# Optimization experiments

Measured on AMD Instinct MI355X. Metric: run time of the kernel, lower is better.

The kernel has to match this reference:

```python
import jax, jax.numpy as jnp
from jax import lax
import numpy as np

B, T, F = 2048, 1000, 40
H1, H2 = 8, 6


def _p(key, shape, fan):
    # uniform(-1/sqrt(fan), 1/sqrt(fan)) like torch LSTM/Linear init
    bound = 1.0 / np.sqrt(fan)
    return jax.random.uniform(key, shape, jnp.float32, -bound, bound)


def setup_inputs() -> dict:
    key = jax.random.key(0)
    ks = jax.random.split(key, 11)
    return {
        "x": jax.random.normal(ks[0], (B, T, F), jnp.float32),
        "W_ih1": _p(ks[1], (4 * H1, F), H1),
        "W_hh1": _p(ks[2], (4 * H1, H1), H1),
        "b_ih1": _p(ks[3], (4 * H1,), H1),
        "b_hh1": _p(ks[4], (4 * H1,), H1),
        "W_ih2": _p(ks[5], (4 * H2, H1), H2),
        "W_hh2": _p(ks[6], (4 * H2, H2), H2),
        "b_ih2": _p(ks[7], (4 * H2,), H2),
        "b_hh2": _p(ks[8], (4 * H2,), H2),
        "W_fc": _p(ks[9], (1, H2), H2),
        "b_fc": _p(ks[10], (1,), H2),
    }


def lstm_layer(x, W_ih, W_hh, b_ih, b_hh):
    """batch_first unidirectional LSTM; returns all hidden states [B,T,H]."""
    Bb = x.shape[0]
    H = W_hh.shape[1]
    # precompute input-side gate preactivations for all timesteps: [T,B,4H]
    xg = (jnp.einsum('btf,gf->btg', x, W_ih) + b_ih + b_hh).transpose(1, 0, 2)
    W_hh_T = W_hh.T  # [H,4H]

    def step(carry, xg_t):
        h, c = carry
        g = xg_t + h @ W_hh_T  # [B,4H]
        i, f, gcell, o = jnp.split(g, 4, axis=-1)  # torch gate order i,f,g,o
        i = jax.nn.sigmoid(i)
        f = jax.nn.sigmoid(f)
        gcell = jnp.tanh(gcell)
        o = jax.nn.sigmoid(o)
        c = f * c + i * gcell
        h = o * jnp.tanh(c)
        return (h, c), h

    h0 = jnp.zeros((Bb, H), x.dtype)
    c0 = jnp.zeros((Bb, H), x.dtype)
    _, hs = lax.scan(step, (h0, c0), xg)  # hs: [T,B,H]
    return hs.transpose(1, 0, 2)


def reference(x, W_ih1, W_hh1, b_ih1, b_hh1, W_ih2, W_hh2, b_ih2, b_hh2, W_fc, b_fc):
    out = lstm_layer(x, W_ih1, W_hh1, b_ih1, b_hh1)
    out = jnp.tanh(out)
    out = lstm_layer(out, W_ih2, W_hh2, b_ih2, b_hh2)
    out = jnp.tanh(out)
    last = out[:, -1, :]  # [B,H2]
    logits = last @ W_fc.T + b_fc  # [B,1]
    return jax.nn.sigmoid(logits)
```

## Files before the change

### kernel.cpp

```cpp
#include <hip/hip_runtime.h>


constexpr int Bn = 2048, Tn = 1000, Fn = 40;
constexpr int H1n = 8, H2n = 6;
constexpr int TT  = 20;
constexpr int NTt = Tn / TT;
constexpr int BW  = 8;

constexpr int SROWF  = TT * Fn + 4;
constexpr int SXF    = BW * SROWF;
constexpr int SXB    = SXF * 4;
constexpr int NCHUNK = (SXB + 1023) / 1024;

__device__ __forceinline__ float frcp(float x) { return __builtin_amdgcn_rcpf(x); }
__device__ __forceinline__ float fsig(float x) { return frcp(1.0f + __expf(-x)); }
__device__ __forceinline__ float ftanh(float x) {
    return fmaf(2.0f, frcp(1.0f + __expf(-2.0f * x)), -1.0f);
}

template <int K>
__device__ __forceinline__ float bswz(float v) {
    return __int_as_float(__builtin_amdgcn_ds_swizzle(__float_as_int(v), (K << 5) | 0x18));
}

__global__ __launch_bounds__(256, 1) void lstm_upl(
    const float* __restrict__ x,
    const float* __restrict__ W_ih1, const float* __restrict__ W_hh1,
    const float* __restrict__ b_ih1, const float* __restrict__ b_hh1,
    const float* __restrict__ W_ih2, const float* __restrict__ W_hh2,
    const float* __restrict__ b_ih2, const float* __restrict__ b_hh2,
    const float* __restrict__ W_fc,  const float* __restrict__ b_fc,
    float* __restrict__ out)
{
    __shared__ float s_x [2][SXF];
    __shared__ float s_xg[2][TT * BW * 32];

    const int lane  = threadIdx.x & 63;
    const int wslot = __builtin_amdgcn_readfirstlane((int)(threadIdx.x >> 6));
    const int b0    = blockIdx.x * BW;


    if (wslot == 0) {
        const int q  = lane >> 3;
        const int j  = lane & 7;
        const int j2 = (j < H2n) ? j : (H2n - 1);

        float wi1[H1n], wf1[H1n], wg1[H1n], wo1[H1n];
#pragma unroll
        for (int k = 0; k < H1n; ++k) {
            wi1[k] = W_hh1[(     j) * H1n + k];
            wf1[k] = W_hh1[( 8 + j) * H1n + k];
            wg1[k] = W_hh1[(16 + j) * H1n + k];
            wo1[k] = W_hh1[(24 + j) * H1n + k];
        }
        float wi2[H1n], wf2[H1n], wg2[H1n], wo2[H1n];
#pragma unroll
        for (int k = 0; k < H1n; ++k) {
            wi2[k] = W_ih2[(     j2) * H1n + k];
            wf2[k] = W_ih2[( 6 + j2) * H1n + k];
            wg2[k] = W_ih2[(12 + j2) * H1n + k];
            wo2[k] = W_ih2[(18 + j2) * H1n + k];
        }
        float vi2[H2n], vf2[H2n], vg2[H2n], vo2[H2n];
#pragma unroll
        for (int k = 0; k < H2n; ++k) {
            vi2[k] = W_hh2[(     j2) * H2n + k];
            vf2[k] = W_hh2[( 6 + j2) * H2n + k];
            vg2[k] = W_hh2[(12 + j2) * H2n + k];
            vo2[k] = W_hh2[(18 + j2) * H2n + k];
        }
        const float bi2c = b_ih2[     j2] + b_hh2[     j2];
        const float bf2c = b_ih2[ 6 + j2] + b_hh2[ 6 + j2];
        const float bg2c = b_ih2[12 + j2] + b_hh2[12 + j2];
        const float bo2c = b_ih2[18 + j2] + b_hh2[18 + j2];

        float wfc[H2n];
#pragma unroll
        for (int k = 0; k < H2n; ++k) wfc[k] = W_fc[k];
        const float bfc = b_fc[0];

        float c1 = 0.f, c2 = 0.f;
        float h1s[H1n], th1s[H1n], h2s[H2n];
#pragma unroll
        for (int k = 0; k < H1n; ++k) { h1s[k] = 0.f; th1s[k] = 0.f; }
#pragma unroll
        for (int k = 0; k < H2n; ++k) h2s[k] = 0.f;

        const int myoff = q * 32 + j * 4;

        for (int p = 0; p <= NTt + 1; ++p) {
            if (p >= 2) {
                const float* xgt = &s_xg[(p - 2) & 1][0];
                float4 xg4 = *(const float4*)(xgt + myoff);
                for (int i = 0; i < TT; ++i) {
                    const int in = (i + 1 < TT) ? (i + 1) : i;
                    const float4 xgn = *(const float4*)(xgt + in * (BW * 32) + myoff);

                    float ai0 = xg4.x, ai1 = 0.f, af0 = xg4.y, af1 = 0.f;
                    float ag0 = xg4.z, ag1 = 0.f, ao0 = xg4.w, ao1 = 0.f;
#pragma unroll
                    for (int k = 0; k < H1n; k += 2) {
                        ai0 = fmaf(h1s[k], wi1[k], ai0); ai1 = fmaf(h1s[k+1], wi1[k+1], ai1);
                        af0 = fmaf(h1s[k], wf1[k], af0); af1 = fmaf(h1s[k+1], wf1[k+1], af1);
                        ag0 = fmaf(h1s[k], wg1[k], ag0); ag1 = fmaf(h1s[k+1], wg1[k+1], ag1);
                        ao0 = fmaf(h1s[k], wo1[k], ao0); ao1 = fmaf(h1s[k+1], wo1[k+1], ao1);
                    }
                    const float iv = fsig (ai0 + ai1);
                    const float fv = fsig (af0 + af1);
                    const float gv = ftanh(ag0 + ag1);
                    const float ov = fsig (ao0 + ao1);
                    c1 = fmaf(fv, c1, iv * gv);
                    const float h1v  = ov * ftanh(c1);
                    const float th1v = ftanh(h1v);

                    h1s[0] = bswz<0>(h1v); h1s[1] = bswz<1>(h1v);
                    h1s[2] = bswz<2>(h1v); h1s[3] = bswz<3>(h1v);
                    h1s[4] = bswz<4>(h1v); h1s[5] = bswz<5>(h1v);
                    h1s[6] = bswz<6>(h1v); h1s[7] = bswz<7>(h1v);
                    th1s[0] = bswz<0>(th1v); th1s[1] = bswz<1>(th1v);
                    th1s[2] = bswz<2>(th1v); th1s[3] = bswz<3>(th1v);
                    th1s[4] = bswz<4>(th1v); th1s[5] = bswz<5>(th1v);
                    th1s[6] = bswz<6>(th1v); th1s[7] = bswz<7>(th1v);

                    float bi0 = bi2c, bi1 = 0.f, bf0 = bf2c, bf1 = 0.f;
                    float bg0 = bg2c, bg1 = 0.f, bo0 = bo2c, bo1 = 0.f;
#pragma unroll
                    for (int k = 0; k < H2n; k += 2) {
                        bi0 = fmaf(h2s[k], vi2[k], bi0); bi1 = fmaf(h2s[k+1], vi2[k+1], bi1);
                        bf0 = fmaf(h2s[k], vf2[k], bf0); bf1 = fmaf(h2s[k+1], vf2[k+1], bf1);
                        bg0 = fmaf(h2s[k], vg2[k], bg0); bg1 = fmaf(h2s[k+1], vg2[k+1], bg1);
                        bo0 = fmaf(h2s[k], vo2[k], bo0); bo1 = fmaf(h2s[k+1], vo2[k+1], bo1);
                    }
#pragma unroll
                    for (int k = 0; k < H1n; k += 2) {
                        bi0 = fmaf(th1s[k], wi2[k], bi0); bi1 = fmaf(th1s[k+1], wi2[k+1], bi1);
                        bf0 = fmaf(th1s[k], wf2[k], bf0); bf1 = fmaf(th1s[k+1], wf2[k+1], bf1);
                        bg0 = fmaf(th1s[k], wg2[k], bg0); bg1 = fmaf(th1s[k+1], wg2[k+1], bg1);
                        bo0 = fmaf(th1s[k], wo2[k], bo0); bo1 = fmaf(th1s[k+1], wo2[k+1], bo1);
                    }
                    const float i2v = fsig (bi0 + bi1);
                    const float f2v = fsig (bf0 + bf1);
                    const float g2v = ftanh(bg0 + bg1);
                    const float o2v = fsig (bo0 + bo1);
                    c2 = fmaf(f2v, c2, i2v * g2v);
                    const float h2v = o2v * ftanh(c2);

                    h2s[0] = bswz<0>(h2v); h2s[1] = bswz<1>(h2v);
                    h2s[2] = bswz<2>(h2v); h2s[3] = bswz<3>(h2v);
                    h2s[4] = bswz<4>(h2v); h2s[5] = bswz<5>(h2v);

                    xg4 = xgn;
                }
            }
            __syncthreads();
        }

        if (j == 0) {
            float a = bfc;
#pragma unroll
            for (int k = 0; k < H2n; ++k) a = fmaf(ftanh(h2s[k]), wfc[k], a);
            out[b0 + q] = fsig(a);
        }
    } else {
        const int wp = wslot - 1;
        const int q  = lane >> 3;
        const int j  = lane & 7;

        float wI[Fn], wF[Fn], wG[Fn], wO[Fn];
#pragma unroll
        for (int k = 0; k < Fn; ++k) {
            wI[k] = W_ih1[(     j) * Fn + k];
            wF[k] = W_ih1[( 8 + j) * Fn + k];
            wG[k] = W_ih1[(16 + j) * Fn + k];
            wO[k] = W_ih1[(24 + j) * Fn + k];
        }
        const float bI = b_ih1[     j] + b_hh1[     j];
        const float bF = b_ih1[ 8 + j] + b_hh1[ 8 + j];
        const float bG = b_ih1[16 + j] + b_hh1[16 + j];
        const float bO = b_ih1[24 + j] + b_hh1[24 + j];

        const char* xcb = (const char*)x;

        for (int p = 0; p <= NTt + 1; ++p) {
            float4 vv[9];
            if (p < NTt) {
#pragma unroll
                for (int ci = 0; ci < 9; ++ci) {
                    const int c = wp + ci * 3;
                    if (c < NCHUNK) {
                        const int o = c * 1024 + lane * 16;
                        if (o < SXB) {
                            const int qq  = o / (SROWF * 4);
                            int       rem = o - qq * (SROWF * 4);
                            if (rem > TT * Fn * 4 - 16) rem = TT * Fn * 4 - 16;
                            vv[ci] = *(const float4*)(xcb
                                       + (size_t)(b0 + qq) * (Tn * Fn * 4)
                                       + (size_t)p * (TT * Fn * 4) + rem);
                        }
                    }
                }
            }

            if (p >= 1 && p <= NTt) {
                const float* xq = &s_x[(p - 1) & 1][0] + q * SROWF;
                float*       so = &s_xg[(p - 1) & 1][0];
                for (int r = wp; r < TT; r += 3) {
                    const float* xr = xq + r * Fn;
                    float i0 = bI, i1 = 0.f, i2 = 0.f, i3 = 0.f;
                    float f0 = bF, f1 = 0.f, f2 = 0.f, f3 = 0.f;
                    float g0 = bG, g1 = 0.f, g2 = 0.f, g3 = 0.f;
                    float o0 = bO, o1 = 0.f, o2 = 0.f, o3 = 0.f;
#pragma unroll
                    for (int k = 0; k < Fn; k += 4) {
                        const float4 cv = *(const float4*)&xr[k];
                        i0 = fmaf(cv.x, wI[k],     i0); i1 = fmaf(cv.y, wI[k + 1], i1);
                        i2 = fmaf(cv.z, wI[k + 2], i2); i3 = fmaf(cv.w, wI[k + 3], i3);
                        f0 = fmaf(cv.x, wF[k],     f0); f1 = fmaf(cv.y, wF[k + 1], f1);
                        f2 = fmaf(cv.z, wF[k + 2], f2); f3 = fmaf(cv.w, wF[k + 3], f3);
                        g0 = fmaf(cv.x, wG[k],     g0); g1 = fmaf(cv.y, wG[k + 1], g1);
                        g2 = fmaf(cv.z, wG[k + 2], g2); g3 = fmaf(cv.w, wG[k + 3], g3);
                        o0 = fmaf(cv.x, wO[k],     o0); o1 = fmaf(cv.y, wO[k + 1], o1);
                        o2 = fmaf(cv.z, wO[k + 2], o2); o3 = fmaf(cv.w, wO[k + 3], o3);
                    }
                    float4 r4;
                    r4.x = (i0 + i1) + (i2 + i3);
                    r4.y = (f0 + f1) + (f2 + f3);
                    r4.z = (g0 + g1) + (g2 + g3);
                    r4.w = (o0 + o1) + (o2 + o3);
                    *(float4*)&so[(r * BW + q) * 32 + j * 4] = r4;
                }
            }

            if (p < NTt) {
                char* ld = (char*)&s_x[p & 1][0];
#pragma unroll
                for (int ci = 0; ci < 9; ++ci) {
                    const int c = wp + ci * 3;
                    if (c < NCHUNK) {
                        const int o = c * 1024 + lane * 16;
                        if (o < SXB) *(float4*)(ld + o) = vv[ci];
                    }
                }
            }
            __syncthreads();
        }
    }
}

extern "C" void kernel_launch(void* const* d_in, const int* in_sizes, int n_in,
                              void* d_out, int out_size, void* d_ws, size_t ws_size,
                              hipStream_t stream) {
    (void)in_sizes; (void)n_in; (void)out_size; (void)d_ws; (void)ws_size;
    const float* x     = (const float*)d_in[0];
    const float* W_ih1 = (const float*)d_in[1];
    const float* W_hh1 = (const float*)d_in[2];
    const float* b_ih1 = (const float*)d_in[3];
    const float* b_hh1 = (const float*)d_in[4];
    const float* W_ih2 = (const float*)d_in[5];
    const float* W_hh2 = (const float*)d_in[6];
    const float* b_ih2 = (const float*)d_in[7];
    const float* b_hh2 = (const float*)d_in[8];
    const float* W_fc  = (const float*)d_in[9];
    const float* b_fc  = (const float*)d_in[10];
    float* out = (float*)d_out;

    lstm_upl<<<dim3(Bn / BW), dim3(256), 0, stream>>>(x, W_ih1, W_hh1, b_ih1, b_hh1,
                                                      W_ih2, W_hh2, b_ih2, b_hh2,
                                                      W_fc, b_fc, out);
}
```

Before: 727.9 us.

## Split LSTM layers across two waves with a shared-memory pipeline stage

The serial recurrence wave is split in two. One wave runs layer 1 and writes tanh(h1) per tile into a new double-buffered shared array, and a second wave runs layer 2 one tile behind. This shortens the per-timestep critical path of each wave, since the layer-1 and layer-2 recurrences now run concurrently. The cost is one fewer producer wave for the input projection (each now loads 13 chunks instead of 9), one more pipeline stage, and extra shared memory.

After: 854.2 us. 17.4% more time.

```diff
diff --git a/kernel.cpp b/kernel.cpp
--- a/kernel.cpp
+++ b/kernel.cpp
@@ -34,6 +34,7 @@
 {
     __shared__ float s_x [2][SXF];
     __shared__ float s_xg[2][TT * BW * 32];
+    __shared__ float s_t1[2][TT * BW * H1n];
 
     const int lane  = threadIdx.x & 63;
     const int wslot = __builtin_amdgcn_readfirstlane((int)(threadIdx.x >> 6));
@@ -41,9 +42,8 @@
 
 
     if (wslot == 0) {
-        const int q  = lane >> 3;
-        const int j  = lane & 7;
-        const int j2 = (j < H2n) ? j : (H2n - 1);
+        const int q = lane >> 3;
+        const int j = lane & 7;
 
         float wi1[H1n], wf1[H1n], wg1[H1n], wo1[H1n];
 #pragma unroll
@@ -53,6 +53,57 @@
             wg1[k] = W_hh1[(16 + j) * H1n + k];
             wo1[k] = W_hh1[(24 + j) * H1n + k];
         }
+
+        float c1 = 0.f;
+        float h1s[H1n];
+#pragma unroll
+        for (int k = 0; k < H1n; ++k) h1s[k] = 0.f;
+
+        const int myoff = q * 32 + j * 4;
+
+        for (int p = 0; p <= NTt + 2; ++p) {
+            if (p >= 2 && p <= NTt + 1) {
+                const int tile = p - 2;
+                const float* xgt = &s_xg[tile & 1][0];
+                float*       t1o = &s_t1[tile & 1][0];
+                float4 xg4 = *(const float4*)(xgt + myoff);
+                for (int i = 0; i < TT; ++i) {
+                    const int in = (i + 1 < TT) ? (i + 1) : i;
+                    const float4 xgn = *(const float4*)(xgt + in * (BW * 32) + myoff);
+
+                    float ai0 = xg4.x, ai1 = 0.f, af0 = xg4.y, af1 = 0.f;
+                    float ag0 = xg4.z, ag1 = 0.f, ao0 = xg4.w, ao1 = 0.f;
+#pragma unroll
+                    for (int k = 0; k < H1n; k += 2) {
+                        ai0 = fmaf(h1s[k], wi1[k], ai0); ai1 = fmaf(h1s[k+1], wi1[k+1], ai1);
+                        af0 = fmaf(h1s[k], wf1[k], af0); af1 = fmaf(h1s[k+1], wf1[k+1], af1);
+                        ag0 = fmaf(h1s[k], wg1[k], ag0); ag1 = fmaf(h1s[k+1], wg1[k+1], ag1);
+                        ao0 = fmaf(h1s[k], wo1[k], ao0); ao1 = fmaf(h1s[k+1], wo1[k+1], ao1);
+                    }
+                    const float iv = fsig (ai0 + ai1);
+                    const float fv = fsig (af0 + af1);
+                    const float gv = ftanh(ag0 + ag1);
+                    const float ov = fsig (ao0 + ao1);
+                    c1 = fmaf(fv, c1, iv * gv);
+                    const float h1v = ov * ftanh(c1);
+
+                    h1s[0] = bswz<0>(h1v); h1s[1] = bswz<1>(h1v);
+                    h1s[2] = bswz<2>(h1v); h1s[3] = bswz<3>(h1v);
+                    h1s[4] = bswz<4>(h1v); h1s[5] = bswz<5>(h1v);
+                    h1s[6] = bswz<6>(h1v); h1s[7] = bswz<7>(h1v);
+
+                    t1o[i * (BW * H1n) + q * H1n + j] = ftanh(h1v);
+
+                    xg4 = xgn;
+                }
+            }
+            __syncthreads();
+        }
+    } else if (wslot == 1) {
+        const int q  = lane >> 3;
+        const int j  = lane & 7;
+        const int j2 = (j < H2n) ? j : (H2n - 1);
+
         float wi2[H1n], wf2[H1n], wg2[H1n], wo2[H1n];
 #pragma unroll
         for (int k = 0; k < H1n; ++k) {
@@ -79,48 +130,26 @@
         for (int k = 0; k < H2n; ++k) wfc[k] = W_fc[k];
         const float bfc = b_fc[0];
 
-        float c1 = 0.f, c2 = 0.f;
-        float h1s[H1n], th1s[H1n], h2s[H2n];
-#pragma unroll
-        for (int k = 0; k < H1n; ++k) { h1s[k] = 0.f; th1s[k] = 0.f; }
+        float c2 = 0.f;
+        float h2s[H2n];
 #pragma unroll
         for (int k = 0; k < H2n; ++k) h2s[k] = 0.f;
 
-        const int myoff = q * 32 + j * 4;
-
-        for (int p = 0; p <= NTt + 1; ++p) {
-            if (p >= 2) {
-                const float* xgt = &s_xg[(p - 2) & 1][0];
-                float4 xg4 = *(const float4*)(xgt + myoff);
+        const int tbase = q * H1n;
+
+        for (int p = 0; p <= NTt + 2; ++p) {
+            if (p >= 3) {
+                const int tile = p - 3;
+                const float* t1 = &s_t1[tile & 1][0];
+                float4 ta = *(const float4*)(t1 + tbase);
+                float4 tb = *(const float4*)(t1 + tbase + 4);
                 for (int i = 0; i < TT; ++i) {
                     const int in = (i + 1 < TT) ? (i + 1) : i;
-                    const float4 xgn = *(const float4*)(xgt + in * (BW * 32) + myoff);
-
-                    float ai0 = xg4.x, ai1 = 0.f, af0 = xg4.y, af1 = 0.f;
-                    float ag0 = xg4.z, ag1 = 0.f, ao0 = xg4.w, ao1 = 0.f;
-#pragma unroll
-                    for (int k = 0; k < H1n; k += 2) {
-                        ai0 = fmaf(h1s[k], wi1[k], ai0); ai1 = fmaf(h1s[k+1], wi1[k+1], ai1);
-                        af0 = fmaf(h1s[k], wf1[k], af0); af1 = fmaf(h1s[k+1], wf1[k+1], af1);
-                        ag0 = fmaf(h1s[k], wg1[k], ag0); ag1 = fmaf(h1s[k+1], wg1[k+1], ag1);
-                        ao0 = fmaf(h1s[k], wo1[k], ao0); ao1 = fmaf(h1s[k+1], wo1[k+1], ao1);
-                    }
-                    const float iv = fsig (ai0 + ai1);
-                    const float fv = fsig (af0 + af1);
-                    const float gv = ftanh(ag0 + ag1);
-                    const float ov = fsig (ao0 + ao1);
-                    c1 = fmaf(fv, c1, iv * gv);
-                    const float h1v  = ov * ftanh(c1);
-                    const float th1v = ftanh(h1v);
-
-                    h1s[0] = bswz<0>(h1v); h1s[1] = bswz<1>(h1v);
-                    h1s[2] = bswz<2>(h1v); h1s[3] = bswz<3>(h1v);
-                    h1s[4] = bswz<4>(h1v); h1s[5] = bswz<5>(h1v);
-                    h1s[6] = bswz<6>(h1v); h1s[7] = bswz<7>(h1v);
-                    th1s[0] = bswz<0>(th1v); th1s[1] = bswz<1>(th1v);
-                    th1s[2] = bswz<2>(th1v); th1s[3] = bswz<3>(th1v);
-                    th1s[4] = bswz<4>(th1v); th1s[5] = bswz<5>(th1v);
-                    th1s[6] = bswz<6>(th1v); th1s[7] = bswz<7>(th1v);
+                    const float4 na = *(const float4*)(t1 + in * (BW * H1n) + tbase);
+                    const float4 nb = *(const float4*)(t1 + in * (BW * H1n) + tbase + 4);
+
+                    const float th1s[H1n] = { ta.x, ta.y, ta.z, ta.w,
+                                              tb.x, tb.y, tb.z, tb.w };
 
                     float bi0 = bi2c, bi1 = 0.f, bf0 = bf2c, bf1 = 0.f;
                     float bg0 = bg2c, bg1 = 0.f, bo0 = bo2c, bo1 = 0.f;
@@ -149,7 +178,7 @@
                     h2s[2] = bswz<2>(h2v); h2s[3] = bswz<3>(h2v);
                     h2s[4] = bswz<4>(h2v); h2s[5] = bswz<5>(h2v);
 
-                    xg4 = xgn;
+                    ta = na; tb = nb;
                 }
             }
             __syncthreads();
@@ -162,7 +191,7 @@
             out[b0 + q] = fsig(a);
         }
     } else {
-        const int wp = wslot - 1;
+        const int wp = wslot - 2;
         const int q  = lane >> 3;
         const int j  = lane & 7;
 
@@ -181,12 +210,12 @@
 
         const char* xcb = (const char*)x;
 
-        for (int p = 0; p <= NTt + 1; ++p) {
-            float4 vv[9];
+        for (int p = 0; p <= NTt + 2; ++p) {
+            float4 vv[13];
             if (p < NTt) {
 #pragma unroll
-                for (int ci = 0; ci < 9; ++ci) {
-                    const int c = wp + ci * 3;
+                for (int ci = 0; ci < 13; ++ci) {
+                    const int c = wp + ci * 2;
                     if (c < NCHUNK) {
                         const int o = c * 1024 + lane * 16;
                         if (o < SXB) {
@@ -204,7 +233,7 @@
             if (p >= 1 && p <= NTt) {
                 const float* xq = &s_x[(p - 1) & 1][0] + q * SROWF;
                 float*       so = &s_xg[(p - 1) & 1][0];
-                for (int r = wp; r < TT; r += 3) {
+                for (int r = wp; r < TT; r += 2) {
                     const float* xr = xq + r * Fn;
                     float i0 = bI, i1 = 0.f, i2 = 0.f, i3 = 0.f;
                     float f0 = bF, f1 = 0.f, f2 = 0.f, f3 = 0.f;
@@ -234,8 +263,8 @@
             if (p < NTt) {
                 char* ld = (char*)&s_x[p & 1][0];
 #pragma unroll
-                for (int ci = 0; ci < 9; ++ci) {
-                    const int c = wp + ci * 3;
+                for (int ci = 0; ci < 13; ++ci) {
+                    const int c = wp + ci * 2;
                     if (c < NCHUNK) {
                         const int o = c * 1024 + lane * 16;
                         if (o < SXB) *(float4*)(ld + o) = vv[ci];
```

## Interleave two independent batch recurrences per recurrence wave with wider batch tiles

Applied to the files above, without the earlier changes.

The recurrence wave now carries two independent batch streams (batch width raised from 8 to 16) and interleaves their layer-1 and layer-2 steps. The aim is to hide the latency of the serial gate/activation/swizzle chain with instruction-level parallelism. The time tile is cut from 20 to 10 so the shared-memory staging still fits, and the producer waves compute input projections for both batch octets. This halves the number of blocks, which leaves more CUs idle, and lengthens each step's instruction stream. Per-step cost may therefore rise more than the ILP saves.

New measurement: 1.053 ms. +44.6%, slower.

```diff
diff --git a/kernel.cpp b/kernel.cpp
--- a/kernel.cpp
+++ b/kernel.cpp
@@ -3,9 +3,9 @@
 
 constexpr int Bn = 2048, Tn = 1000, Fn = 40;
 constexpr int H1n = 8, H2n = 6;
-constexpr int TT  = 20;
-constexpr int NTt = Tn / TT;
-constexpr int BW  = 8;
+constexpr int TT  = 10;
+constexpr int NTp = Tn / TT;
+constexpr int BW  = 16;
 
 constexpr int SROWF  = TT * Fn + 4;
 constexpr int SXF    = BW * SROWF;
@@ -21,6 +21,79 @@
 template <int K>
 __device__ __forceinline__ float bswz(float v) {
     return __int_as_float(__builtin_amdgcn_ds_swizzle(__float_as_int(v), (K << 5) | 0x18));
+}
+
+struct Stream {
+    float c1, c2;
+    float h1s[H1n], th1s[H1n], h2s[H2n];
+};
+
+__device__ __forceinline__ void l1_step(
+    Stream& s, const float4& xg4,
+    const float (&wi1)[H1n], const float (&wf1)[H1n],
+    const float (&wg1)[H1n], const float (&wo1)[H1n])
+{
+    float ai0 = xg4.x, ai1 = 0.f, af0 = xg4.y, af1 = 0.f;
+    float ag0 = xg4.z, ag1 = 0.f, ao0 = xg4.w, ao1 = 0.f;
+#pragma unroll
+    for (int k = 0; k < H1n; k += 2) {
+        ai0 = fmaf(s.h1s[k], wi1[k], ai0); ai1 = fmaf(s.h1s[k+1], wi1[k+1], ai1);
+        af0 = fmaf(s.h1s[k], wf1[k], af0); af1 = fmaf(s.h1s[k+1], wf1[k+1], af1);
+        ag0 = fmaf(s.h1s[k], wg1[k], ag0); ag1 = fmaf(s.h1s[k+1], wg1[k+1], ag1);
+        ao0 = fmaf(s.h1s[k], wo1[k], ao0); ao1 = fmaf(s.h1s[k+1], wo1[k+1], ao1);
+    }
+    const float iv = fsig (ai0 + ai1);
+    const float fv = fsig (af0 + af1);
+    const float gv = ftanh(ag0 + ag1);
+    const float ov = fsig (ao0 + ao1);
+    s.c1 = fmaf(fv, s.c1, iv * gv);
+    const float h1v  = ov * ftanh(s.c1);
+    const float th1v = ftanh(h1v);
+
+    s.h1s[0] = bswz<0>(h1v);  s.h1s[1] = bswz<1>(h1v);
+    s.h1s[2] = bswz<2>(h1v);  s.h1s[3] = bswz<3>(h1v);
+    s.h1s[4] = bswz<4>(h1v);  s.h1s[5] = bswz<5>(h1v);
+    s.h1s[6] = bswz<6>(h1v);  s.h1s[7] = bswz<7>(h1v);
+    s.th1s[0] = bswz<0>(th1v); s.th1s[1] = bswz<1>(th1v);
+    s.th1s[2] = bswz<2>(th1v); s.th1s[3] = bswz<3>(th1v);
+    s.th1s[4] = bswz<4>(th1v); s.th1s[5] = bswz<5>(th1v);
+    s.th1s[6] = bswz<6>(th1v); s.th1s[7] = bswz<7>(th1v);
+}
+
+__device__ __forceinline__ void l2_step(
+    Stream& s,
+    const float (&wi2)[H1n], const float (&wf2)[H1n],
+    const float (&wg2)[H1n], const float (&wo2)[H1n],
+    const float (&vi2)[H2n], const float (&vf2)[H2n],
+    const float (&vg2)[H2n], const float (&vo2)[H2n],
+    float bi2c, float bf2c, float bg2c, float bo2c)
+{
+    float bi0 = bi2c, bi1 = 0.f, bf0 = bf2c, bf1 = 0.f;
+    float bg0 = bg2c, bg1 = 0.f, bo0 = bo2c, bo1 = 0.f;
+#pragma unroll
+    for (int k = 0; k < H2n; k += 2) {
+        bi0 = fmaf(s.h2s[k], vi2[k], bi0); bi1 = fmaf(s.h2s[k+1], vi2[k+1], bi1);
+        bf0 = fmaf(s.h2s[k], vf2[k], bf0); bf1 = fmaf(s.h2s[k+1], vf2[k+1], bf1);
+        bg0 = fmaf(s.h2s[k], vg2[k], bg0); bg1 = fmaf(s.h2s[k+1], vg2[k+1], bg1);
+        bo0 = fmaf(s.h2s[k], vo2[k], bo0); bo1 = fmaf(s.h2s[k+1], vo2[k+1], bo1);
+    }
+#pragma unroll
+    for (int k = 0; k < H1n; k += 2) {
+        bi0 = fmaf(s.th1s[k], wi2[k], bi0); bi1 = fmaf(s.th1s[k+1], wi2[k+1], bi1);
+        bf0 = fmaf(s.th1s[k], wf2[k], bf0); bf1 = fmaf(s.th1s[k+1], wf2[k+1], bf1);
+        bg0 = fmaf(s.th1s[k], wg2[k], bg0); bg1 = fmaf(s.th1s[k+1], wg2[k+1], bg1);
+        bo0 = fmaf(s.th1s[k], wo2[k], bo0); bo1 = fmaf(s.th1s[k+1], wo2[k+1], bo1);
+    }
+    const float i2v = fsig (bi0 + bi1);
+    const float f2v = fsig (bf0 + bf1);
+    const float g2v = ftanh(bg0 + bg1);
+    const float o2v = fsig (bo0 + bo1);
+    s.c2 = fmaf(f2v, s.c2, i2v * g2v);
+    const float h2v = o2v * ftanh(s.c2);
+
+    s.h2s[0] = bswz<0>(h2v); s.h2s[1] = bswz<1>(h2v);
+    s.h2s[2] = bswz<2>(h2v); s.h2s[3] = bswz<3>(h2v);
+    s.h2s[4] = bswz<4>(h2v); s.h2s[5] = bswz<5>(h2v);
 }
 
 __global__ __launch_bounds__(256, 1) void lstm_upl(
@@ -79,87 +152,51 @@
         for (int k = 0; k < H2n; ++k) wfc[k] = W_fc[k];
         const float bfc = b_fc[0];
 
-        float c1 = 0.f, c2 = 0.f;
-        float h1s[H1n], th1s[H1n], h2s[H2n];
-#pragma unroll
-        for (int k = 0; k < H1n; ++k) { h1s[k] = 0.f; th1s[k] = 0.f; }
-#pragma unroll
-        for (int k = 0; k < H2n; ++k) h2s[k] = 0.f;
-
-        const int myoff = q * 32 + j * 4;
-
-        for (int p = 0; p <= NTt + 1; ++p) {
+        Stream sA, sB;
+        sA.c1 = sA.c2 = sB.c1 = sB.c2 = 0.f;
+#pragma unroll
+        for (int k = 0; k < H1n; ++k) {
+            sA.h1s[k] = sA.th1s[k] = 0.f;
+            sB.h1s[k] = sB.th1s[k] = 0.f;
+        }
+#pragma unroll
+        for (int k = 0; k < H2n; ++k) { sA.h2s[k] = 0.f; sB.h2s[k] = 0.f; }
+
+        const int offA = (    q) * 32 + j * 4;
+        const int offB = (8 + q) * 32 + j * 4;
+
+        for (int p = 0; p <= NTp + 1; ++p) {
             if (p >= 2) {
                 const float* xgt = &s_xg[(p - 2) & 1][0];
-                float4 xg4 = *(const float4*)(xgt + myoff);
+                float4 xga = *(const float4*)(xgt + offA);
+                float4 xgb = *(const float4*)(xgt + offB);
                 for (int i = 0; i < TT; ++i) {
                     const int in = (i + 1 < TT) ? (i + 1) : i;
-                    const float4 xgn = *(const float4*)(xgt + in * (BW * 32) + myoff);
-
-                    float ai0 = xg4.x, ai1 = 0.f, af0 = xg4.y, af1 = 0.f;
-                    float ag0 = xg4.z, ag1 = 0.f, ao0 = xg4.w, ao1 = 0.f;
-#pragma unroll
-                    for (int k = 0; k < H1n; k += 2) {
-                        ai0 = fmaf(h1s[k], wi1[k], ai0); ai1 = fmaf(h1s[k+1], wi1[k+1], ai1);
-                        af0 = fmaf(h1s[k], wf1[k], af0); af1 = fmaf(h1s[k+1], wf1[k+1], af1);
-                        ag0 = fmaf(h1s[k], wg1[k], ag0); ag1 = fmaf(h1s[k+1], wg1[k+1], ag1);
-                        ao0 = fmaf(h1s[k], wo1[k], ao0); ao1 = fmaf(h1s[k+1], wo1[k+1], ao1);
-                    }
-                    const float iv = fsig (ai0 + ai1);
-                    const float fv = fsig (af0 + af1);
-                    const float gv = ftanh(ag0 + ag1);
-                    const float ov = fsig (ao0 + ao1);
-                    c1 = fmaf(fv, c1, iv * gv);
-                    const float h1v  = ov * ftanh(c1);
-                    const float th1v = ftanh(h1v);
-
-                    h1s[0] = bswz<0>(h1v); h1s[1] = bswz<1>(h1v);
-                    h1s[2] = bswz<2>(h1v); h1s[3] = bswz<3>(h1v);
-                    h1s[4] = bswz<4>(h1v); h1s[5] = bswz<5>(h1v);
-                    h1s[6] = bswz<6>(h1v); h1s[7] = bswz<7>(h1v);
-                    th1s[0] = bswz<0>(th1v); th1s[1] = bswz<1>(th1v);
-                    th1s[2] = bswz<2>(th1v); th1s[3] = bswz<3>(th1v);
-                    th1s[4] = bswz<4>(th1v); th1s[5] = bswz<5>(th1v);
-                    th1s[6] = bswz<6>(th1v); th1s[7] = bswz<7>(th1v);
-
-                    float bi0 = bi2c, bi1 = 0.f, bf0 = bf2c, bf1 = 0.f;
-                    float bg0 = bg2c, bg1 = 0.f, bo0 = bo2c, bo1 = 0.f;
-#pragma unroll
-                    for (int k = 0; k < H2n; k += 2) {
-                        bi0 = fmaf(h2s[k], vi2[k], bi0); bi1 = fmaf(h2s[k+1], vi2[k+1], bi1);
-                        bf0 = fmaf(h2s[k], vf2[k], bf0); bf1 = fmaf(h2s[k+1], vf2[k+1], bf1);
-                        bg0 = fmaf(h2s[k], vg2[k], bg0); bg1 = fmaf(h2s[k+1], vg2[k+1], bg1);
-                        bo0 = fmaf(h2s[k], vo2[k], bo0); bo1 = fmaf(h2s[k+1], vo2[k+1], bo1);
-                    }
-#pragma unroll
-                    for (int k = 0; k < H1n; k += 2) {
-                        bi0 = fmaf(th1s[k], wi2[k], bi0); bi1 = fmaf(th1s[k+1], wi2[k+1], bi1);
-                        bf0 = fmaf(th1s[k], wf2[k], bf0); bf1 = fmaf(th1s[k+1], wf2[k+1], bf1);
-                        bg0 = fmaf(th1s[k], wg2[k], bg0); bg1 = fmaf(th1s[k+1], wg2[k+1], bg1);
-                        bo0 = fmaf(th1s[k], wo2[k], bo0); bo1 = fmaf(th1s[k+1], wo2[k+1], bo1);
-                    }
-                    const float i2v = fsig (bi0 + bi1);
-                    const float f2v = fsig (bf0 + bf1);
-                    const float g2v = ftanh(bg0 + bg1);
-                    const float o2v = fsig (bo0 + bo1);
-                    c2 = fmaf(f2v, c2, i2v * g2v);
-                    const float h2v = o2v * ftanh(c2);
-
-                    h2s[0] = bswz<0>(h2v); h2s[1] = bswz<1>(h2v);
-                    h2s[2] = bswz<2>(h2v); h2s[3] = bswz<3>(h2v);
-                    h2s[4] = bswz<4>(h2v); h2s[5] = bswz<5>(h2v);
-
-                    xg4 = xgn;
+                    const float4 xna = *(const float4*)(xgt + in * (BW * 32) + offA);
+                    const float4 xnb = *(const float4*)(xgt + in * (BW * 32) + offB);
+
+                    l1_step(sA, xga, wi1, wf1, wg1, wo1);
+                    l1_step(sB, xgb, wi1, wf1, wg1, wo1);
+                    l2_step(sA, wi2, wf2, wg2, wo2, vi2, vf2, vg2, vo2,
+                            bi2c, bf2c, bg2c, bo2c);
+                    l2_step(sB, wi2, wf2, wg2, wo2, vi2, vf2, vg2, vo2,
+                            bi2c, bf2c, bg2c, bo2c);
+
+                    xga = xna; xgb = xnb;
                 }
             }
             __syncthreads();
         }
 
         if (j == 0) {
-            float a = bfc;
-#pragma unroll
-            for (int k = 0; k < H2n; ++k) a = fmaf(ftanh(h2s[k]), wfc[k], a);
-            out[b0 + q] = fsig(a);
+            float a = bfc, b = bfc;
+#pragma unroll
+            for (int k = 0; k < H2n; ++k) {
+                a = fmaf(ftanh(sA.h2s[k]), wfc[k], a);
+                b = fmaf(ftanh(sB.h2s[k]), wfc[k], b);
+            }
+            out[b0 + q]     = fsig(a);
+            out[b0 + 8 + q] = fsig(b);
         }
     } else {
         const int wp = wslot - 1;
@@ -181,9 +218,9 @@
 
         const char* xcb = (const char*)x;
 
-        for (int p = 0; p <= NTt + 1; ++p) {
+        for (int p = 0; p <= NTp + 1; ++p) {
             float4 vv[9];
-            if (p < NTt) {
+            if (p < NTp) {
 #pragma unroll
                 for (int ci = 0; ci < 9; ++ci) {
                     const int c = wp + ci * 3;
@@ -201,37 +238,42 @@
                 }
             }
 
-            if (p >= 1 && p <= NTt) {
-                const float* xq = &s_x[(p - 1) & 1][0] + q * SROWF;
-                float*       so = &s_xg[(p - 1) & 1][0];
-                for (int r = wp; r < TT; r += 3) {
-                    const float* xr = xq + r * Fn;
-                    float i0 = bI, i1 = 0.f, i2 = 0.f, i3 = 0.f;
-                    float f0 = bF, f1 = 0.f, f2 = 0.f, f3 = 0.f;
-                    float g0 = bG, g1 = 0.f, g2 = 0.f, g3 = 0.f;
-                    float o0 = bO, o1 = 0.f, o2 = 0.f, o3 = 0.f;
-#pragma unroll
-                    for (int k = 0; k < Fn; k += 4) {
-                        const float4 cv = *(const float4*)&xr[k];
-                        i0 = fmaf(cv.x, wI[k],     i0); i1 = fmaf(cv.y, wI[k + 1], i1);
-                        i2 = fmaf(cv.z, wI[k + 2], i2); i3 = fmaf(cv.w, wI[k + 3], i3);
-                        f0 = fmaf(cv.x, wF[k],     f0); f1 = fmaf(cv.y, wF[k + 1], f1);
-                        f2 = fmaf(cv.z, wF[k + 2], f2); f3 = fmaf(cv.w, wF[k + 3], f3);
-                        g0 = fmaf(cv.x, wG[k],     g0); g1 = fmaf(cv.y, wG[k + 1], g1);
-                        g2 = fmaf(cv.z, wG[k + 2], g2); g3 = fmaf(cv.w, wG[k + 3], g3);
-                        o0 = fmaf(cv.x, wO[k],     o0); o1 = fmaf(cv.y, wO[k + 1], o1);
-                        o2 = fmaf(cv.z, wO[k + 2], o2); o3 = fmaf(cv.w, wO[k + 3], o3);
+            if (p >= 1 && p <= NTp) {
+                const float* sxb = &s_x[(p - 1) & 1][0];
+                float*       so  = &s_xg[(p - 1) & 1][0];
+#pragma unroll
+                for (int oct = 0; oct < 2; ++oct) {
+                    const int bb = oct * 8 + q;
+                    const float* xq = sxb + bb * SROWF;
+                    for (int r = wp; r < TT; r += 3) {
+                        const float* xr = xq + r * Fn;
+                        float i0 = bI, i1 = 0.f, i2 = 0.f, i3 = 0.f;
+                        float f0 = bF, f1 = 0.f, f2 = 0.f, f3 = 0.f;
+                        float g0 = bG, g1 = 0.f, g2 = 0.f, g3 = 0.f;
+                        float o0 = bO, o1 = 0.f, o2 = 0.f, o3 = 0.f;
+#pragma unroll
+                        for (int k = 0; k < Fn; k += 4) {
+                            const float4 cv = *(const float4*)&xr[k];
+                            i0 = fmaf(cv.x, wI[k],     i0); i1 = fmaf(cv.y, wI[k + 1], i1);
+                            i2 = fmaf(cv.z, wI[k + 2], i2); i3 = fmaf(cv.w, wI[k + 3], i3);
+                            f0 = fmaf(cv.x, wF[k],     f0); f1 = fmaf(cv.y, wF[k + 1], f1);
+                            f2 = fmaf(cv.z, wF[k + 2], f2); f3 = fmaf(cv.w, wF[k + 3], f3);
+                            g0 = fmaf(cv.x, wG[k],     g0); g1 = fmaf(cv.y, wG[k + 1], g1);
+                            g2 = fmaf(cv.z, wG[k + 2], g2); g3 = fmaf(cv.w, wG[k + 3], g3);
+                            o0 = fmaf(cv.x, wO[k],     o0); o1 = fmaf(cv.y, wO[k + 1], o1);
+                            o2 = fmaf(cv.z, wO[k + 2], o2); o3 = fmaf(cv.w, wO[k + 3], o3);
+                        }
+                        float4 r4;
+                        r4.x = (i0 + i1) + (i2 + i3);
+                        r4.y = (f0 + f1) + (f2 + f3);
+                        r4.z = (g0 + g1) + (g2 + g3);
+                        r4.w = (o0 + o1) + (o2 + o3);
+                        *(float4*)&so[(r * BW + bb) * 32 + j * 4] = r4;
                     }
-                    float4 r4;
-                    r4.x = (i0 + i1) + (i2 + i3);
-                    r4.y = (f0 + f1) + (f2 + f3);
-                    r4.z = (g0 + g1) + (g2 + g3);
-                    r4.w = (o0 + o1) + (o2 + o3);
-                    *(float4*)&so[(r * BW + q) * 32 + j * 4] = r4;
                 }
             }
 
-            if (p < NTt) {
+            if (p < NTp) {
                 char* ld = (char*)&s_x[p & 1][0];
 #pragma unroll
                 for (int ci = 0; ci < 9; ++ci) {
```
